# Kernel optimization log

Hardware: AMD Instinct MI355X
Metric: run time of the kernel (lower is better)

Reference implementation:

```python
import jax, jax.numpy as jnp
import numpy as np

N, M, E, D = 20000, 1024, 640000, 256


def setup_inputs() -> dict:
    key = jax.random.key(0)
    ks = jax.random.split(key, 24)
    mask = jax.random.uniform(ks[0], (N, M)) < 0.05
    init = jnp.where(mask, jax.random.uniform(ks[1], (N, M), minval=0.1, maxval=1.0), 0.0)
    inp = {
        'init': init,
        'ei_cc': jax.random.randint(ks[2], (2, E), 0, N, dtype=jnp.int32),
        'ei_cac': jax.random.randint(ks[3], (2, E), 0, N, dtype=jnp.int32),
        'ei_csc': jax.random.randint(ks[4], (2, E), 0, N, dtype=jnp.int32),
        'ea_cc': jax.random.uniform(ks[5], (E,), minval=0.1, maxval=1.0),
        'ea_cac': jax.random.uniform(ks[6], (E,), minval=0.1, maxval=1.0),
        'ea_csc': jax.random.uniform(ks[7], (E,), minval=0.1, maxval=1.0),
        # Projection MLP: Linear(1,16) -> ReLU -> Linear(16,D)
        'pW1': jax.random.normal(ks[8], (1, 16)) * 0.5,
        'pb1': jnp.zeros((16,)),
        'pW2': jax.random.normal(ks[9], (16, D)) * 0.1,
        'pb2': jnp.zeros((D,)),
        # three GCN branches, 3 layers each (all D->D)
        'W_cc': jax.random.normal(ks[10], (3, D, D)) * 0.05,
        'b_cc': jnp.zeros((3, D)),
        'W_cac': jax.random.normal(ks[11], (3, D, D)) * 0.05,
        'b_cac': jnp.zeros((3, D)),
        'W_csc': jax.random.normal(ks[12], (3, D, D)) * 0.05,
        'b_csc': jnp.zeros((3, D)),
        # meta-path attention: Linear(D, 1)
        'w_att': jax.random.normal(ks[13], (D,)) * 0.05,
        'b_att': jnp.zeros((1,)),
    }
    return inp


def projection(init, pW1, pb1, pW2, pb2):
    # torch code feeds the *indices* of nonzero columns through the MLP and
    # mean-pools per row. Vectorize: precompute MLP(j) for every column index j,
    # then masked mean.
    idx = jnp.arange(M, dtype=init.dtype)[:, None]          # [M, 1]
    h = jax.nn.relu(idx @ pW1 + pb1)                        # [M, 16]
    col_emb = h @ pW2 + pb2                                 # [M, D]
    mask = (init != 0).astype(init.dtype)                   # [N, M]
    cnt = mask.sum(axis=1)                                  # [N]
    emb = (mask @ col_emb) / jnp.maximum(cnt, 1.0)[:, None]
    return jnp.where(cnt[:, None] > 0, emb, 0.0)            # zero rows stay zero


def gcn_conv(x, edge_index, edge_weight, W, b):
    # PyG GCNConv with edge_weight: add self loops (w=1), symmetric norm.
    n = x.shape[0]
    loop = jnp.arange(n, dtype=edge_index.dtype)
    row = jnp.concatenate([edge_index[0], loop])
    col = jnp.concatenate([edge_index[1], loop])
    w = jnp.concatenate([edge_weight, jnp.ones((n,), x.dtype)])
    deg = jax.ops.segment_sum(w, col, num_segments=n)
    dinv = jnp.where(deg > 0, jax.lax.rsqrt(deg), 0.0)
    norm = dinv[row] * w * dinv[col]                        # [E+N]
    h = x @ W                                               # [N, D]
    out = jax.ops.segment_sum(norm[:, None] * h[row], col, num_segments=n)
    return out + b


def gcn_branch(x, edge_index, edge_weight, Ws, bs):
    for l in range(3):
        x = jax.nn.relu(gcn_conv(x, edge_index, edge_weight, Ws[l], bs[l]))
    return x


def reference(init, ei_cc, ei_cac, ei_csc, ea_cc, ea_cac, ea_csc,
              pW1, pb1, pW2, pb2, W_cc, b_cc, W_cac, b_cac, W_csc, b_csc,
              w_att, b_att):
    x0 = projection(init, pW1, pb1, pW2, pb2)               # [N, D]
    out_cc = gcn_branch(x0, ei_cc, ea_cc, W_cc, b_cc)
    out_cac = gcn_branch(x0, ei_cac, ea_cac, W_cac, b_cac)
    out_csc = gcn_branch(x0, ei_csc, ea_csc, W_csc, b_csc)
    emb = jnp.stack([out_cc, out_cac, out_csc], axis=0)     # [3, N, D]
    scores = jnp.einsum('pnd,d->pn', emb, w_att) + b_att[0] # [3, N]
    attn = jax.nn.softmax(scores, axis=0)                   # softmax over meta-paths
    return jnp.einsum('pn,pnd->nd', attn, emb)              # [N, D]
```

## Files before the change

kernel.cpp:

```cpp
#include <hip/hip_runtime.h>
#include <hip/hip_bf16.h>

typedef __hip_bfloat16 bf16;
typedef __bf16 v8bf __attribute__((ext_vector_type(8)));
typedef float f32x4 __attribute__((ext_vector_type(4)));
typedef unsigned int v4u __attribute__((ext_vector_type(4)));

constexpr int N = 20000, M = 1024, E = 640000, D = 256;
constexpr size_t SEGEL = (size_t)N * D;
constexpr int NCHUNK = 10000;
constexpr int NSLICE = 64;
constexpr int ESLICE = E / NSLICE;

__device__ __forceinline__ float b2f(bf16 v) { return __bfloat162float(v); }
__device__ __forceinline__ bf16 f2b(float f) { return __float2bfloat16(f); }
__device__ __forceinline__ float u2f(unsigned short u) { return __uint_as_float(((unsigned)u) << 16); }
__device__ __forceinline__ unsigned short f2u(float f) { bf16 h = __float2bfloat16(f); return *(unsigned short*)&h; }
__device__ __forceinline__ float loadf(const void* p, size_t i, int isbf) {
    return isbf ? b2f(((const bf16*)p)[i]) : ((const float*)p)[i];
}
__device__ __forceinline__ void fma8(float* acc, uint4 v, float w) {
    acc[0] = fmaf(w, u2f((unsigned short)(v.x & 0xffffu)), acc[0]);
    acc[1] = fmaf(w, u2f((unsigned short)(v.x >> 16)), acc[1]);
    acc[2] = fmaf(w, u2f((unsigned short)(v.y & 0xffffu)), acc[2]);
    acc[3] = fmaf(w, u2f((unsigned short)(v.y >> 16)), acc[3]);
    acc[4] = fmaf(w, u2f((unsigned short)(v.z & 0xffffu)), acc[4]);
    acc[5] = fmaf(w, u2f((unsigned short)(v.z >> 16)), acc[5]);
    acc[6] = fmaf(w, u2f((unsigned short)(v.w & 0xffffu)), acc[6]);
    acc[7] = fmaf(w, u2f((unsigned short)(v.w >> 16)), acc[7]);
}
__device__ __forceinline__ void add8(float* a, uint4 v) {
    a[0] += u2f((unsigned short)(v.x & 0xffffu));
    a[1] += u2f((unsigned short)(v.x >> 16));
    a[2] += u2f((unsigned short)(v.y & 0xffffu));
    a[3] += u2f((unsigned short)(v.y >> 16));
    a[4] += u2f((unsigned short)(v.z & 0xffffu));
    a[5] += u2f((unsigned short)(v.z >> 16));
    a[6] += u2f((unsigned short)(v.w & 0xffffu));
    a[7] += u2f((unsigned short)(v.w >> 16));
}
__device__ __forceinline__ unsigned pack2(float a, float b) {
    return (unsigned)f2u(a) | ((unsigned)f2u(b) << 16);
}

__global__ void detect_kernel(const void* __restrict__ ea, int* __restrict__ flag)
{
    if (threadIdx.x == 0 && blockIdx.x == 0) {
        const unsigned short* u = (const unsigned short*)ea;
        int cnt = 0;
        for (int i = 0; i < 64; i++) {
            float f = __uint_as_float(((unsigned)u[i]) << 16);
            if (f >= 0.05f && f <= 1.05f) cnt++;
        }
        *flag = (cnt >= 60) ? 1 : 0;
    }
}

__global__ __launch_bounds__(256) void prep_kernel(
    const void* __restrict__ W0, const void* __restrict__ W1, const void* __restrict__ W2,
    const void* __restrict__ pW1, const void* __restrict__ pb1,
    const void* __restrict__ pW2, const void* __restrict__ pb2,
    bf16* __restrict__ WT, bf16* __restrict__ cemb, const int* __restrict__ flag)
{
    int isbf = *flag;
    int b = blockIdx.x;
    if (b < 2304) {
        int mat = b >> 8, n = b & 255, k = threadIdx.x;
        const void* W = (mat < 3) ? W0 : (mat < 6) ? W1 : W2;
        int lm = mat - (mat < 3 ? 0 : (mat < 6 ? 3 : 6));
        WT[(size_t)mat * 65536 + n * 256 + k] =
            f2b(loadf(W, (size_t)lm * 65536 + k * 256 + n, isbf));
    } else {
        int j = b - 2304;
        int d = threadIdx.x;
        float jf = (float)j;
        float acc = loadf(pb2, d, isbf);
        #pragma unroll
        for (int k = 0; k < 16; k++) {
            float h = fmaxf(jf * loadf(pW1, k, isbf) + loadf(pb1, k, isbf), 0.0f);
            acc += h * loadf(pW2, k * 256 + d, isbf);
        }
        cemb[(size_t)j * 256 + d] = f2b(acc);
    }
}

__global__ __launch_bounds__(256) void projection_kernel(
    const void* __restrict__ init, const bf16* __restrict__ cemb,
    bf16* __restrict__ x0, const int* __restrict__ flag)
{
    __shared__ unsigned short idxs[4][1024];
    int isbf = *flag;
    int wave = threadIdx.x >> 6, lane = threadIdx.x & 63;
    int i = blockIdx.x * 4 + wave;
    unsigned long long below = (lane == 63) ? 0x7fffffffffffffffull
                                            : ((1ull << lane) - 1ull);
    int cnt = 0;
    if (isbf) {
        const unsigned short* row = (const unsigned short*)init + (size_t)i * 1024;
        for (int c0 = 0; c0 < 1024; c0 += 64) {
            bool nz = (row[c0 + lane] & 0x7fffu) != 0;
            unsigned long long m = __ballot(nz);
            if (nz) idxs[wave][cnt + __popcll(m & below)] = (unsigned short)(c0 + lane);
            cnt += __popcll(m);
        }
    } else {
        const float* row = (const float*)init + (size_t)i * 1024;
        for (int c0 = 0; c0 < 1024; c0 += 64) {
            bool nz = row[c0 + lane] != 0.0f;
            unsigned long long m = __ballot(nz);
            if (nz) idxs[wave][cnt + __popcll(m & below)] = (unsigned short)(c0 + lane);
            cnt += __popcll(m);
        }
    }
    const uint4* cr4 = (const uint4*)cemb;
    int L = lane & 31, h = lane >> 5;
    float acc[8] = {0.f, 0.f, 0.f, 0.f, 0.f, 0.f, 0.f, 0.f};
    int npair = cnt >> 1;
    int t = 0;
    for (; t + 8 <= npair; t += 8) {
        uint4 v0 = cr4[(size_t)idxs[wave][2 * (t + 0) + h] * 32 + L];
        uint4 v1 = cr4[(size_t)idxs[wave][2 * (t + 1) + h] * 32 + L];
        uint4 v2 = cr4[(size_t)idxs[wave][2 * (t + 2) + h] * 32 + L];
        uint4 v3 = cr4[(size_t)idxs[wave][2 * (t + 3) + h] * 32 + L];
        uint4 v4 = cr4[(size_t)idxs[wave][2 * (t + 4) + h] * 32 + L];
        uint4 v5 = cr4[(size_t)idxs[wave][2 * (t + 5) + h] * 32 + L];
        uint4 v6 = cr4[(size_t)idxs[wave][2 * (t + 6) + h] * 32 + L];
        uint4 v7 = cr4[(size_t)idxs[wave][2 * (t + 7) + h] * 32 + L];
        add8(acc, v0); add8(acc, v1); add8(acc, v2); add8(acc, v3);
        add8(acc, v4); add8(acc, v5); add8(acc, v6); add8(acc, v7);
    }
    for (; t < npair; t++) {
        uint4 v = cr4[(size_t)idxs[wave][2 * t + h] * 32 + L];
        add8(acc, v);
    }
    if ((cnt & 1) && h == 0) {
        uint4 v = cr4[(size_t)idxs[wave][cnt - 1] * 32 + L];
        add8(acc, v);
    }
    #pragma unroll
    for (int j = 0; j < 8; j++) acc[j] += __shfl_xor(acc[j], 32, 64);
    if (h == 0) {
        float rinv = 1.0f / fmaxf((float)cnt, 1.0f);
        v4u o;
        o.x = pack2(acc[0] * rinv, acc[1] * rinv);
        o.y = pack2(acc[2] * rinv, acc[3] * rinv);
        o.z = pack2(acc[4] * rinv, acc[5] * rinv);
        o.w = pack2(acc[6] * rinv, acc[7] * rinv);
        ((v4u*)x0)[(size_t)i * 32 + L] = o;
    }
}

__global__ __launch_bounds__(256) void countP_kernel(
    const int* __restrict__ e0, const int* __restrict__ e1, const int* __restrict__ e2,
    int* __restrict__ P)
{
    __shared__ int cur[NCHUNK];
    int b = blockIdx.x;
    int pb = b >> 7, rem = b & 127;
    int ck = rem >> 6, s = rem & 63;
    const int* ei = pb == 0 ? e0 : pb == 1 ? e1 : e2;
    int c0 = ck * NCHUNK;
    int t = threadIdx.x;
    for (int i = t; i < NCHUNK; i += 256) cur[i] = 0;
    __syncthreads();
    int ebase = s * ESLICE;
    for (int e = ebase + t; e < ebase + ESLICE; e += 256) {
        int c = ei[E + e];
        if (c >= c0 && c < c0 + NCHUNK) atomicAdd(&cur[c - c0], 1);
    }
    __syncthreads();
    int* Prow = P + ((size_t)(pb * NSLICE + s)) * N + c0;
    for (int i = t; i < NCHUNK; i += 256) Prow[i] = cur[i];
}

__global__ __launch_bounds__(256) void cnt_sum_kernel(
    const int* __restrict__ P, int* __restrict__ cnt)
{
    int id = blockIdx.x * 256 + threadIdx.x;
    if (id >= 3 * N) return;
    int pb = id / N, c = id - pb * N;
    int sum = 0;
    #pragma unroll 8
    for (int s = 0; s < NSLICE; s++)
        sum += P[((size_t)(pb * NSLICE + s)) * N + c];
    cnt[id] = sum;
}

__global__ __launch_bounds__(1024) void scan_kernel(
    const int* __restrict__ cnt, int* __restrict__ col_ptr)
{
    int pb = blockIdx.x;
    int base = pb * E;
    __shared__ int s[1024];
    int t = threadIdx.x;
    const int CH = 20;
    int i0 = t * CH;
    int sum = 0;
    for (int j = 0; j < CH; j++) { int i = i0 + j; if (i < N) sum += cnt[pb * N + i]; }
    s[t] = sum;
    __syncthreads();
    for (int off = 1; off < 1024; off <<= 1) {
        int v = (t >= off) ? s[t - off] : 0;
        __syncthreads();
        s[t] += v;
        __syncthreads();
    }
    int run = base + s[t] - sum;
    for (int j = 0; j < CH; j++) {
        int i = i0 + j;
        if (i < N) {
            col_ptr[pb * (N + 1) + i] = run;
            run += cnt[pb * N + i];
        }
    }
    if (t == 0) col_ptr[pb * (N + 1) + N] = base + E;
}

__global__ __launch_bounds__(256) void base_kernel(
    int* __restrict__ P, const int* __restrict__ col_ptr)
{
    int id = blockIdx.x * 256 + threadIdx.x;
    if (id >= 3 * N) return;
    int pb = id / N, c = id - pb * N;
    int run = col_ptr[pb * (N + 1) + c];
    for (int s = 0; s < NSLICE; s++) {
        size_t idx = ((size_t)(pb * NSLICE + s)) * N + c;
        int v = P[idx];
        P[idx] = run;
        run += v;
    }
}

__global__ __launch_bounds__(256) void fill_kernel(
    const int* __restrict__ e0, const int* __restrict__ e1, const int* __restrict__ e2,
    const void* __restrict__ a0, const void* __restrict__ a1, const void* __restrict__ a2,
    const int* __restrict__ P, int2* __restrict__ epack, const int* __restrict__ flag)
{
    __shared__ int cur[NCHUNK];
    int isbf = *flag;
    int b = blockIdx.x;
    int pb = b >> 7, rem = b & 127;
    int ck = rem >> 6, s = rem & 63;
    const int* ei = pb == 0 ? e0 : pb == 1 ? e1 : e2;
    const void* ea = pb == 0 ? a0 : pb == 1 ? a1 : a2;
    int c0 = ck * NCHUNK;
    int t = threadIdx.x;
    const int* Prow = P + ((size_t)(pb * NSLICE + s)) * N + c0;
    for (int i = t; i < NCHUNK; i += 256) cur[i] = Prow[i];
    __syncthreads();
    int ebase = s * ESLICE;
    for (int e = ebase + t; e < ebase + ESLICE; e += 256) {
        int c = ei[E + e];
        if (c >= c0 && c < c0 + NCHUNK) {
            int r = ei[e];
            float w = loadf(ea, e, isbf);
            int pos = atomicAdd(&cur[c - c0], 1);
            int2 v; v.x = r; v.y = __float_as_int(w);
            epack[pos] = v;
        }
    }
}

__global__ __launch_bounds__(256) void degsum_kernel(
    const int* __restrict__ col_ptr, const int2* __restrict__ epack,
    float* __restrict__ dinv, float* __restrict__ nloop)
{
    int wave = threadIdx.x >> 6, lane = threadIdx.x & 63;
    int pb = blockIdx.x / 5000;
    int i = (blockIdx.x - pb * 5000) * 4 + wave;
    int start = col_ptr[pb * (N + 1) + i], end = col_ptr[pb * (N + 1) + i + 1];
    float sum = 0.0f;
    for (int p = start + lane; p < end; p += 64) sum += __int_as_float(epack[p].y);
    for (int off = 1; off < 64; off <<= 1) sum += __shfl_xor(sum, off, 64);
    if (lane == 0) {
        float dg = 1.0f + sum;
        dinv[pb * N + i] = rsqrtf(dg);
        nloop[pb * N + i] = 1.0f / dg;
    }
}

__global__ __launch_bounds__(256) void snorm_sort_kernel(
    const int* __restrict__ col_ptr, int2* __restrict__ epack,
    const float* __restrict__ dinv)
{
    int wave = threadIdx.x >> 6, lane = threadIdx.x & 63;
    int pb = blockIdx.x / 5000;
    int i = (blockIdx.x - pb * 5000) * 4 + wave;
    int start = col_ptr[pb * (N + 1) + i], end = col_ptr[pb * (N + 1) + i + 1];
    float dc = dinv[pb * N + i];
    for (int base = start; base < end; base += 64) {
        int n = end - base; n = n < 64 ? n : 64;
        int key = 0x7fffffff, val = 0;
        if (lane < n) {
            int2 v = epack[base + lane];
            key = v.x;
            val = __float_as_int(dc * __int_as_float(v.y) * dinv[pb * N + v.x]);
        }
        #pragma unroll
        for (int k = 2; k <= 64; k <<= 1) {
            #pragma unroll
            for (int j = k >> 1; j > 0; j >>= 1) {
                int pk = __shfl_xor(key, j, 64);
                int pv = __shfl_xor(val, j, 64);
                bool up = (lane & k) == 0;
                bool lower = (lane & j) == 0;
                bool takeMin = (up == lower);
                bool sw = takeMin ? (pk < key) : (pk > key);
                if (sw) { key = pk; val = pv; }
            }
        }
        if (lane < n) {
            int2 o; o.x = key; o.y = val;
            epack[base + lane] = o;
        }
    }
}

__global__ __launch_bounds__(256) void aggregate_kernel(
    const bf16* __restrict__ xi0, const bf16* __restrict__ xi1, const bf16* __restrict__ xi2,
    bf16* __restrict__ yb,
    const int* __restrict__ col_ptr, const int2* __restrict__ epack,
    const float* __restrict__ nloop)
{
    int wave = threadIdx.x >> 6, lane = threadIdx.x & 63;
    int pb = blockIdx.x / 5000;
    int i = (blockIdx.x - pb * 5000) * 4 + wave;
    const bf16* x = pb == 0 ? xi0 : pb == 1 ? xi1 : xi2;
    const uint4* xr = (const uint4*)x;
    int L = lane & 31, h = lane >> 5;
    int start = col_ptr[pb * (N + 1) + i], end = col_ptr[pb * (N + 1) + i + 1];
    float nl = nloop[pb * N + i];
    float acc[8];
    {
        uint4 sv = xr[(size_t)i * 32 + L];
        float self = (h == 0) ? nl : 0.0f;
        #pragma unroll
        for (int j = 0; j < 8; j++) acc[j] = 0.0f;
        fma8(acc, sv, self);
    }
    for (int base = start; base < end; base += 64) {
        int n = end - base; n = n < 64 ? n : 64;
        int ex = 0, ey = 0;
        if (lane < n) {
            unsigned long long ev = __builtin_nontemporal_load(
                (const unsigned long long*)(epack + base + lane));
            ex = (int)(unsigned)(ev & 0xffffffffull);
            ey = (int)(unsigned)(ev >> 32);
        }
        int pmax = (n + 1) >> 1;
        for (int p0 = 0; p0 < pmax; p0 += 8) {
            int m = pmax - p0; m = m < 8 ? m : 8;
            uint4 v[8];
            float w[8];
            #pragma unroll
            for (int k = 0; k < 8; k++) {
                int e = 2 * (p0 + k) + h;
                int rj = __shfl(ex, e, 64);
                w[k] = __int_as_float(__shfl(ey, e, 64));
                if (k < m) v[k] = xr[(size_t)rj * 32 + L];
            }
            #pragma unroll
            for (int k = 0; k < 8; k++)
                if (k < m) fma8(acc, v[k], w[k]);
        }
    }
    #pragma unroll
    for (int j = 0; j < 8; j++) acc[j] += __shfl_xor(acc[j], 32, 64);
    if (h == 0) {
        v4u o;
        o.x = pack2(acc[0], acc[1]);
        o.y = pack2(acc[2], acc[3]);
        o.z = pack2(acc[4], acc[5]);
        o.w = pack2(acc[6], acc[7]);
        __builtin_nontemporal_store(o,
            (v4u*)yb + (size_t)pb * (SEGEL / 8) + (size_t)i * 32 + L);
    }
}

__global__ __launch_bounds__(256) void gemm_relu_kernel(
    const bf16* __restrict__ yb, const bf16* __restrict__ WT, int layer,
    const void* __restrict__ b0, const void* __restrict__ b1, const void* __restrict__ b2,
    bf16* __restrict__ o0, bf16* __restrict__ o1, bf16* __restrict__ o2,
    const int* __restrict__ flag)
{
    int isbf = *flag;
    int pl = blockIdx.x / 625, blk = blockIdx.x - pl * 625;
    const bf16* y = yb + (size_t)pl * SEGEL;
    const bf16* wt = WT + (size_t)(pl * 3 + layer) * 65536;
    const void* bias = pl == 0 ? b0 : pl == 1 ? b1 : b2;
    bf16* xout = pl == 0 ? o0 : pl == 1 ? o1 : o2;

    int wave = threadIdx.x >> 6, lane = threadIdx.x & 63;
    int m0 = blk * 32 + (wave >> 1) * 16;
    int n0 = (wave & 1) * 128;
    int mrow = lane & 15, q = lane >> 4;

    f32x4 acc[8] = {};
    const v8bf* arow = reinterpret_cast<const v8bf*>(y + (size_t)(m0 + mrow) * 256);
    for (int k0 = 0; k0 < 256; k0 += 32) {
        v8bf a = arow[(k0 >> 3) + q];
        #pragma unroll
        for (int nt = 0; nt < 8; nt++) {
            const v8bf* brow = reinterpret_cast<const v8bf*>(wt + (size_t)(n0 + nt * 16 + mrow) * 256);
            acc[nt] = __builtin_amdgcn_mfma_f32_16x16x32_bf16(a, brow[(k0 >> 3) + q], acc[nt], 0, 0, 0);
        }
    }
    #pragma unroll
    for (int nt = 0; nt < 8; nt++) {
        int col = n0 + nt * 16 + mrow;
        float bv = loadf(bias, (size_t)layer * 256 + col, isbf);
        #pragma unroll
        for (int r = 0; r < 4; r++) {
            int row = m0 + q * 4 + r;
            xout[(size_t)row * 256 + col] = f2b(fmaxf(acc[nt][r] + bv, 0.0f));
        }
    }
}

__global__ __launch_bounds__(768) void gemm_attn_kernel(
    const bf16* __restrict__ yb, const bf16* __restrict__ WT,
    const void* __restrict__ b0, const void* __restrict__ b1, const void* __restrict__ b2,
    const void* __restrict__ w_att, void* __restrict__ out,
    const int* __restrict__ flag)
{
    __shared__ float sc[3][32];
    __shared__ unsigned short semb[3][32][256];
    int isbf = *flag;
    int blk = blockIdx.x;
    int tid = threadIdx.x;
    int wave = tid >> 6, lane = tid & 63;
    int p  = wave >> 2;
    int wm = (wave >> 1) & 1;
    int wn = wave & 1;
    int m0 = blk * 32 + wm * 16;
    int n0 = wn * 128;
    int mrow = lane & 15, q = lane >> 4;

    if (tid < 96) ((float*)sc)[tid] = 0.0f;
    __syncthreads();

    {
        const bf16* y = yb + (size_t)p * SEGEL;
        const bf16* wt = WT + (size_t)(p * 3 + 2) * 65536;
        const void* bias = p == 0 ? b0 : p == 1 ? b1 : b2;
        f32x4 acc[8] = {};
        const v8bf* arow = reinterpret_cast<const v8bf*>(y + (size_t)(m0 + mrow) * 256);
        for (int k0 = 0; k0 < 256; k0 += 32) {
            v8bf a = arow[(k0 >> 3) + q];
            #pragma unroll
            for (int nt = 0; nt < 8; nt++) {
                const v8bf* brow = reinterpret_cast<const v8bf*>(wt + (size_t)(n0 + nt * 16 + mrow) * 256);
                acc[nt] = __builtin_amdgcn_mfma_f32_16x16x32_bf16(a, brow[(k0 >> 3) + q], acc[nt], 0, 0, 0);
            }
        }
        float part[4] = {0.0f, 0.0f, 0.0f, 0.0f};
        #pragma unroll
        for (int nt = 0; nt < 8; nt++) {
            int col = n0 + nt * 16 + mrow;
            float bv = loadf(bias, (size_t)2 * 256 + col, isbf);
            float wv = loadf(w_att, col, isbf);
            #pragma unroll
            for (int r = 0; r < 4; r++) {
                int lrow = wm * 16 + q * 4 + r;
                unsigned short eu = f2u(fmaxf(acc[nt][r] + bv, 0.0f));
                semb[p][lrow][col] = eu;
                part[r] = fmaf(u2f(eu), wv, part[r]);
            }
        }
        #pragma unroll
        for (int off = 1; off < 16; off <<= 1) {
            #pragma unroll
            for (int r = 0; r < 4; r++) part[r] += __shfl_xor(part[r], off, 64);
        }
        if (mrow == 0) {
            #pragma unroll
            for (int r = 0; r < 4; r++)
                atomicAdd(&sc[p][wm * 16 + q * 4 + r], part[r]);
        }
    }
    __syncthreads();
    if (tid < 32) {
        float s0 = sc[0][tid], s1 = sc[1][tid], s2 = sc[2][tid];
        float mx = fmaxf(s0, fmaxf(s1, s2));
        float a0 = expf(s0 - mx), a1 = expf(s1 - mx), a2 = expf(s2 - mx);
        float inv = 1.0f / (a0 + a1 + a2);
        sc[0][tid] = a0 * inv; sc[1][tid] = a1 * inv; sc[2][tid] = a2 * inv;
    }
    __syncthreads();
    for (int idx = tid; idx < 32 * 256; idx += 768) {
        int lrow = idx >> 8, col = idx & 255;
        float v = sc[0][lrow] * u2f(semb[0][lrow][col])
                + sc[1][lrow] * u2f(semb[1][lrow][col])
                + sc[2][lrow] * u2f(semb[2][lrow][col]);
        size_t o = (size_t)(blk * 32 + lrow) * 256 + col;
        if (isbf) ((bf16*)out)[o] = f2b(v);
        else      ((float*)out)[o] = v;
    }
}

extern "C" void kernel_launch(void* const* d_in, const int* in_sizes, int n_in,
                              void* d_out, int out_size, void* d_ws, size_t ws_size,
                              hipStream_t stream)
{
    (void)in_sizes; (void)n_in; (void)out_size; (void)ws_size;

    const void* init = d_in[0];
    const int*  ei[3] = {(const int*)d_in[1], (const int*)d_in[2], (const int*)d_in[3]};
    const void* ea[3] = {d_in[4], d_in[5], d_in[6]};
    const void* pW1 = d_in[7];
    const void* pb1 = d_in[8];
    const void* pW2 = d_in[9];
    const void* pb2 = d_in[10];
    const void* Wb[3] = {d_in[11], d_in[13], d_in[15]};
    const void* bb[3] = {d_in[12], d_in[14], d_in[16]};
    const void* w_att = d_in[17];

    char* ws = (char*)d_ws;
    size_t off = 0;
    auto carve = [&](size_t bytes) -> char* {
        off = (off + 255) & ~(size_t)255;
        char* p = ws + off; off += bytes; return p;
    };
    int*   flag  = (int*)carve(4);
    bf16*  WT    = (bf16*)carve((size_t)9 * 65536 * 2);
    bf16*  cemb  = (bf16*)carve((size_t)M * D * 2);
    bf16*  x0    = (bf16*)carve(SEGEL * 2);
    int*   cnt   = (int*)carve((size_t)3 * N * 4);
    int*   colp  = (int*)carve((size_t)3 * (N + 1) * 4);
    float* dinv  = (float*)carve((size_t)3 * N * 4);
    float* nloop = (float*)carve((size_t)3 * N * 4);
    int2*  epack = (int2*)carve((size_t)3 * E * 8);
    bf16*  ybuf  = (bf16*)carve((size_t)3 * SEGEL * 2);
    bf16*  bufA  = (bf16*)carve((size_t)3 * SEGEL * 2);
    bf16*  bufB  = (bf16*)carve((size_t)3 * SEGEL * 2);
    int* P = (int*)bufB;

    detect_kernel<<<1, 64, 0, stream>>>(ea[0], flag);
    prep_kernel<<<3328, 256, 0, stream>>>(Wb[0], Wb[1], Wb[2],
                                          pW1, pb1, pW2, pb2, WT, cemb, flag);
    projection_kernel<<<5000, 256, 0, stream>>>(init, cemb, x0, flag);

    countP_kernel<<<384, 256, 0, stream>>>(ei[0], ei[1], ei[2], P);
    cnt_sum_kernel<<<(3 * N + 255) / 256, 256, 0, stream>>>(P, cnt);
    scan_kernel<<<3, 1024, 0, stream>>>(cnt, colp);
    base_kernel<<<(3 * N + 255) / 256, 256, 0, stream>>>(P, colp);
    fill_kernel<<<384, 256, 0, stream>>>(ei[0], ei[1], ei[2], ea[0], ea[1], ea[2],
                                         P, epack, flag);
    degsum_kernel<<<15000, 256, 0, stream>>>(colp, epack, dinv, nloop);
    snorm_sort_kernel<<<15000, 256, 0, stream>>>(colp, epack, dinv);

    const bf16 *i0 = x0, *i1 = x0, *i2 = x0;
    for (int l = 0; l < 3; l++) {
        aggregate_kernel<<<15000, 256, 0, stream>>>(i0, i1, i2, ybuf, colp, epack, nloop);
        if (l < 2) {
            bf16* dst = (l == 0) ? bufA : bufB;
            gemm_relu_kernel<<<1875, 256, 0, stream>>>(ybuf, WT, l, bb[0], bb[1], bb[2],
                                                       dst, dst + SEGEL, dst + 2 * SEGEL, flag);
            i0 = dst; i1 = dst + SEGEL; i2 = dst + 2 * SEGEL;
        } else {
            gemm_attn_kernel<<<625, 768, 0, stream>>>(ybuf, WT, bb[0], bb[1], bb[2],
                                                      w_att, d_out, flag);
        }
    }
}
```

Measured before the change: 882.2 us.

## Vectorize projection nonzero scan and split aggregate launches per branch

The projection kernel now reads each row of the interaction matrix with 16-byte vector loads. It builds per-lane nonzero bitmasks and computes write offsets with a shuffle-based prefix scan instead of one ballot per 64 scalars. Separately, the aggregate kernel is launched three times per layer, once per meta-path, with a single input pointer instead of selecting the branch inside the kernel. This is meant to cut load instructions in the scan, and to keep each launch's gather working set to one feature matrix for better cache locality. It adds a block-wide barrier, a longer shuffle scan, and two extra kernel launches per layer.

```diff
diff --git a/kernel.cpp b/kernel.cpp
--- a/kernel.cpp
+++ b/kernel.cpp
@@ -92,26 +92,61 @@
     int isbf = *flag;
     int wave = threadIdx.x >> 6, lane = threadIdx.x & 63;
     int i = blockIdx.x * 4 + wave;
-    unsigned long long below = (lane == 63) ? 0x7fffffffffffffffull
-                                            : ((1ull << lane) - 1ull);
     int cnt = 0;
     if (isbf) {
-        const unsigned short* row = (const unsigned short*)init + (size_t)i * 1024;
-        for (int c0 = 0; c0 < 1024; c0 += 64) {
-            bool nz = (row[c0 + lane] & 0x7fffu) != 0;
-            unsigned long long m = __ballot(nz);
-            if (nz) idxs[wave][cnt + __popcll(m & below)] = (unsigned short)(c0 + lane);
-            cnt += __popcll(m);
+        const uint4* row = (const uint4*)((const unsigned short*)init + (size_t)i * 1024);
+        #pragma unroll
+        for (int it = 0; it < 2; it++) {
+            uint4 v = row[it * 64 + lane];
+            int c0 = it * 512 + lane * 8;
+            unsigned nz = 0;
+            nz |= ((v.x & 0x00007fffu) != 0) ? 1u   : 0;
+            nz |= ((v.x & 0x7fff0000u) != 0) ? 2u   : 0;
+            nz |= ((v.y & 0x00007fffu) != 0) ? 4u   : 0;
+            nz |= ((v.y & 0x7fff0000u) != 0) ? 8u   : 0;
+            nz |= ((v.z & 0x00007fffu) != 0) ? 16u  : 0;
+            nz |= ((v.z & 0x7fff0000u) != 0) ? 32u  : 0;
+            nz |= ((v.w & 0x00007fffu) != 0) ? 64u  : 0;
+            nz |= ((v.w & 0x7fff0000u) != 0) ? 128u : 0;
+            int cl = __popc(nz);
+            int s = cl;
+            #pragma unroll
+            for (int off = 1; off < 64; off <<= 1) {
+                int t = __shfl(s, lane - off, 64);
+                if (lane >= off) s += t;
+            }
+            int o = cnt + s - cl;
+            #pragma unroll
+            for (int j = 0; j < 8; j++)
+                if (nz & (1u << j)) idxs[wave][o++] = (unsigned short)(c0 + j);
+            cnt += __shfl(s, 63, 64);
         }
     } else {
-        const float* row = (const float*)init + (size_t)i * 1024;
-        for (int c0 = 0; c0 < 1024; c0 += 64) {
-            bool nz = row[c0 + lane] != 0.0f;
-            unsigned long long m = __ballot(nz);
-            if (nz) idxs[wave][cnt + __popcll(m & below)] = (unsigned short)(c0 + lane);
-            cnt += __popcll(m);
-        }
-    }
+        const float4* row = (const float4*)((const float*)init + (size_t)i * 1024);
+        #pragma unroll
+        for (int it = 0; it < 4; it++) {
+            float4 v = row[it * 64 + lane];
+            int c0 = it * 256 + lane * 4;
+            unsigned nz = 0;
+            if (v.x != 0.0f) nz |= 1u;
+            if (v.y != 0.0f) nz |= 2u;
+            if (v.z != 0.0f) nz |= 4u;
+            if (v.w != 0.0f) nz |= 8u;
+            int cl = __popc(nz);
+            int s = cl;
+            #pragma unroll
+            for (int off = 1; off < 64; off <<= 1) {
+                int t = __shfl(s, lane - off, 64);
+                if (lane >= off) s += t;
+            }
+            int o = cnt + s - cl;
+            #pragma unroll
+            for (int j = 0; j < 4; j++)
+                if (nz & (1u << j)) idxs[wave][o++] = (unsigned short)(c0 + j);
+            cnt += __shfl(s, 63, 64);
+        }
+    }
+    __syncthreads();
     const uint4* cr4 = (const uint4*)cemb;
     int L = lane & 31, h = lane >> 5;
     float acc[8] = {0.f, 0.f, 0.f, 0.f, 0.f, 0.f, 0.f, 0.f};
@@ -317,15 +352,12 @@
 }
 
 __global__ __launch_bounds__(256) void aggregate_kernel(
-    const bf16* __restrict__ xi0, const bf16* __restrict__ xi1, const bf16* __restrict__ xi2,
-    bf16* __restrict__ yb,
+    const bf16* __restrict__ x, bf16* __restrict__ yb,
     const int* __restrict__ col_ptr, const int2* __restrict__ epack,
-    const float* __restrict__ nloop)
+    const float* __restrict__ nloop, int pb)
 {
     int wave = threadIdx.x >> 6, lane = threadIdx.x & 63;
-    int pb = blockIdx.x / 5000;
-    int i = (blockIdx.x - pb * 5000) * 4 + wave;
-    const bf16* x = pb == 0 ? xi0 : pb == 1 ? xi1 : xi2;
+    int i = blockIdx.x * 4 + wave;
     const uint4* xr = (const uint4*)x;
     int L = lane & 31, h = lane >> 5;
     int start = col_ptr[pb * (N + 1) + i], end = col_ptr[pb * (N + 1) + i + 1];
@@ -551,7 +583,10 @@
 
     const bf16 *i0 = x0, *i1 = x0, *i2 = x0;
     for (int l = 0; l < 3; l++) {
-        aggregate_kernel<<<15000, 256, 0, stream>>>(i0, i1, i2, ybuf, colp, epack, nloop);
+        const bf16* xin[3] = {i0, i1, i2};
+        for (int pb = 0; pb < 3; pb++)
+            aggregate_kernel<<<5000, 256, 0, stream>>>(xin[pb], ybuf, colp, epack,
+                                                       nloop, pb);
         if (l < 2) {
             bf16* dst = (l == 0) ? bufA : bufB;
             gemm_relu_kernel<<<1875, 256, 0, stream>>>(ybuf, WT, l, bb[0], bb[1], bb[2],
```

Result: no change. 898.3 us (+1.8%).
